# Performance work log

Measured on AMD Instinct MI355X. Metric: run time of the kernel, lower is better.

Reference implementation:

```python
import jax, jax.numpy as jnp
import numpy as np

MAX_ITER = 10
TAU = 1.0


def setup_inputs() -> dict:
    key = jax.random.key(0)
    k1, k2, k3 = jax.random.split(key, 3)
    B, R, C = 64, 1024, 1024
    s = jax.random.normal(k1, (B, R, C), dtype=jnp.float32)
    # nrows <= ncols per batch => no transposed_batch branch in the original
    nrows = jax.random.randint(k2, (B,), 128, 512).astype(jnp.int32)
    ncols = jax.random.randint(k3, (B,), 512, C + 1).astype(jnp.int32)
    return {"s": s, "nrows": nrows, "ncols": ncols}


def _masked_lse(x, mask, axis):
    """logsumexp over `axis` restricted to mask==True; finite-safe everywhere.
    Equivalent to torch.logsumexp after writing -inf into masked-out entries,
    but keeps all values finite so grads are clean."""
    neg = jnp.asarray(-1e30, x.dtype)
    m = jax.lax.stop_gradient(jnp.max(jnp.where(mask, x, neg), axis=axis, keepdims=True))
    e = jnp.where(mask, jnp.exp(jnp.where(mask, x, m) - m), jnp.zeros((), x.dtype))
    sum_e = jnp.sum(e, axis=axis, keepdims=True)
    any_m = jnp.any(mask, axis=axis, keepdims=True)
    return m + jnp.log(jnp.where(any_m, sum_e, jnp.ones((), x.dtype)))


def _sinkhorn(s, nrows, ncols):
    B, R, C = s.shape
    row_mask = (jnp.arange(R)[None, :] < nrows[:, None])[:, :, None]  # [B,R,1]
    col_mask = (jnp.arange(C)[None, :] < ncols[:, None])[:, None, :]  # [B,1,C]
    valid = row_mask & col_mask                                        # [B,R,C]
    log_s = s / TAU
    # Alternating row/col normalization in log space. In the original, entries
    # outside [nrows,ncols] are set to -inf and ignored by logsumexp; here we
    # keep them finite and mask inside the logsumexp, which is the same math
    # on the valid region, and we zero the invalid region at the end (exp(-inf)=0).
    for i in range(MAX_ITER):
        if i % 2 == 0:  # row normalization
            lse = _masked_lse(log_s, valid, axis=2)          # [B,R,1]
            log_s = log_s - jnp.where(row_mask, lse, 0.0)
        else:           # col normalization
            lse = _masked_lse(log_s, valid, axis=1)          # [B,1,C]
            log_s = log_s - jnp.where(col_mask, lse, 0.0)
    return jnp.where(valid, jnp.exp(log_s), jnp.zeros((), s.dtype))


def reference(s, nrows, ncols):
    return _sinkhorn(s, nrows, ncols)
```

## Files before the change

### kernel.cpp

```cpp
#include <hip/hip_runtime.h>
#include <hip/hip_fp16.h>


#define B_DIM 64

__device__ __forceinline__ float fast_rcp(float x) {
#if __has_builtin(__builtin_amdgcn_rcpf)
    return __builtin_amdgcn_rcpf(x);
#else
    return 1.0f / x;
#endif
}

__device__ __forceinline__ float wave_sum(float x) {
    #pragma unroll
    for (int off = 1; off < 64; off <<= 1) x += __shfl_xor(x, off);
    return x;
}


__device__ __forceinline__ void phase2_col(
    const __half* __restrict__ E, const float* a_lds, int b, int r0, int nr,
    int nc, int t, float* __restrict__ cs_cur)
{
    if (r0 >= nr) return;
    const int c0 = t << 1;
    if (c0 >= nc) return;
    const int rend = min(r0 + 64, nr);
    const __half* __restrict__ Eb = E + ((size_t)b << 19) + c0;

    float sA0 = 0.f, sA1 = 0.f, sB0 = 0.f, sB1 = 0.f;
    int r = r0;
    for (; r + 4 <= rend; r += 4) {
        const float2 f0 = __half22float2(*reinterpret_cast<const __half2*>(Eb + ((size_t)(r + 0) << 10)));
        const float2 f1 = __half22float2(*reinterpret_cast<const __half2*>(Eb + ((size_t)(r + 1) << 10)));
        const float2 f2 = __half22float2(*reinterpret_cast<const __half2*>(Eb + ((size_t)(r + 2) << 10)));
        const float2 f3 = __half22float2(*reinterpret_cast<const __half2*>(Eb + ((size_t)(r + 3) << 10)));
        const float a0 = a_lds[r + 0 - r0], a1 = a_lds[r + 1 - r0];
        const float a2 = a_lds[r + 2 - r0], a3 = a_lds[r + 3 - r0];
        sA0 = fmaf(f0.x, a0, sA0); sA1 = fmaf(f0.y, a0, sA1);
        sB0 = fmaf(f1.x, a1, sB0); sB1 = fmaf(f1.y, a1, sB1);
        sA0 = fmaf(f2.x, a2, sA0); sA1 = fmaf(f2.y, a2, sA1);
        sB0 = fmaf(f3.x, a3, sB0); sB1 = fmaf(f3.y, a3, sB1);
    }
    for (; r < rend; ++r) {
        const float2 f = __half22float2(*reinterpret_cast<const __half2*>(Eb + ((size_t)r << 10)));
        const float av = a_lds[r - r0];
        sA0 = fmaf(f.x, av, sA0); sA1 = fmaf(f.y, av, sA1);
    }
    atomicAdd(cs_cur + (b << 10) + c0, sA0 + sB0);
    if (c0 + 1 < nc)
        atomicAdd(cs_cur + (b << 10) + c0 + 1, sA1 + sB1);
}

__global__ __launch_bounds__(512) void pair_first(
    const float* __restrict__ s, const int* __restrict__ nrows,
    const int* __restrict__ ncols, __half* __restrict__ E,
    float* __restrict__ a, float* __restrict__ cs_cur,
    float* __restrict__ cs_next)
{
    const int b = blockIdx.y;
    const int rc = blockIdx.x;
    const int t = threadIdx.x;
    if (t < 128) cs_next[(b << 10) + (rc << 7) + t] = 0.f;

    const int nr = nrows[b];
    const int nc = ncols[b];
    const int r0 = rc << 6;
    __shared__ float a_lds[64];

    const int wave = t >> 6;
    const int lane = t & 63;
    const int cbase = lane << 4;
    const int nv = min(max(nc - cbase, 0), 16);

    if (r0 < nr) {
        #pragma unroll 1
        for (int k = 0; k < 8; ++k) {
            const int r = r0 + (wave << 3) + k;
            float s0 = 0.f, s1 = 0.f;
            if (r < nr) {
                const float* __restrict__ srow =
                    s + ((size_t)b << 20) + ((size_t)r << 10) + cbase;
                __half* __restrict__ erow =
                    E + ((size_t)b << 19) + ((size_t)r << 10) + cbase;
                float e[16];
                #pragma unroll
                for (int q = 0; q < 4; ++q) {
                    const float4 x = *reinterpret_cast<const float4*>(srow + (q << 2));
                    e[4 * q + 0] = __expf(x.x); e[4 * q + 1] = __expf(x.y);
                    e[4 * q + 2] = __expf(x.z); e[4 * q + 3] = __expf(x.w);
                }
                __half2 h[8];
                #pragma unroll
                for (int q = 0; q < 8; ++q)
                    h[q] = __floats2half2_rn(e[2 * q], e[2 * q + 1]);
                *reinterpret_cast<float4*>(erow)     = *reinterpret_cast<float4*>(&h[0]);
                *reinterpret_cast<float4*>(erow + 8) = *reinterpret_cast<float4*>(&h[4]);
                #pragma unroll
                for (int j = 0; j < 16; j += 2) {
                    s0 += (j < nv) ? e[j] : 0.f;
                    s1 += (j + 1 < nv) ? e[j + 1] : 0.f;
                }
            }
            const float sum = wave_sum(s0 + s1);
            if (lane == 0) a_lds[(wave << 3) + k] = (r < nr) ? 1.0f / sum : 0.f;
        }
    } else if (t < 64) {
        a_lds[t] = 0.f;
    }
    __syncthreads();
    if (t < 64) a[(b << 9) + r0 + t] = a_lds[t];

    phase2_col(E, a_lds, b, r0, nr, nc, t, cs_cur);
}

__global__ __launch_bounds__(512) void pair_mid(
    const __half* __restrict__ E, const int* __restrict__ nrows,
    const int* __restrict__ ncols, const float* __restrict__ cs_prev,
    float* __restrict__ a, float* __restrict__ cs_cur,
    float* __restrict__ cs_next)
{
    const int b = blockIdx.y;
    const int rc = blockIdx.x;
    const int t = threadIdx.x;
    if (t < 128) cs_next[(b << 10) + (rc << 7) + t] = 0.f;

    const int nr = nrows[b];
    const int nc = ncols[b];
    const int r0 = rc << 6;
    __shared__ float a_lds[64];

    const int wave = t >> 6;
    const int lane = t & 63;
    const int cbase = lane << 4;

    if (r0 < nr) {
        float w[16];
        const float* __restrict__ csp = cs_prev + (b << 10) + cbase;
        #pragma unroll
        for (int q = 0; q < 4; ++q) {
            const float4 c4 = *reinterpret_cast<const float4*>(csp + (q << 2));
            w[4 * q + 0] = (cbase + 4 * q + 0 < nc) ? fast_rcp(c4.x) : 0.f;
            w[4 * q + 1] = (cbase + 4 * q + 1 < nc) ? fast_rcp(c4.y) : 0.f;
            w[4 * q + 2] = (cbase + 4 * q + 2 < nc) ? fast_rcp(c4.z) : 0.f;
            w[4 * q + 3] = (cbase + 4 * q + 3 < nc) ? fast_rcp(c4.w) : 0.f;
        }
        #pragma unroll 1
        for (int k = 0; k < 8; ++k) {
            const int r = r0 + (wave << 3) + k;
            float s0 = 0.f, s1 = 0.f;
            if (r < nr) {
                const __half* __restrict__ erow =
                    E + ((size_t)b << 19) + ((size_t)r << 10) + cbase;
                float4 p0 = *reinterpret_cast<const float4*>(erow);
                float4 p1 = *reinterpret_cast<const float4*>(erow + 8);
                const __half2* h0 = reinterpret_cast<const __half2*>(&p0);
                const __half2* h1 = reinterpret_cast<const __half2*>(&p1);
                #pragma unroll
                for (int q = 0; q < 4; ++q) {
                    const float2 f = __half22float2(h0[q]);
                    s0 = fmaf(f.x, w[2 * q], s0);
                    s1 = fmaf(f.y, w[2 * q + 1], s1);
                }
                #pragma unroll
                for (int q = 0; q < 4; ++q) {
                    const float2 f = __half22float2(h1[q]);
                    s0 = fmaf(f.x, w[8 + 2 * q], s0);
                    s1 = fmaf(f.y, w[8 + 2 * q + 1], s1);
                }
            }
            const float sum = wave_sum(s0 + s1);
            if (lane == 0) a_lds[(wave << 3) + k] = (r < nr) ? 1.0f / sum : 0.f;
        }
    } else if (t < 64) {
        a_lds[t] = 0.f;
    }
    __syncthreads();
    if (t < 64) a[(b << 9) + r0 + t] = a_lds[t];

    phase2_col(E, a_lds, b, r0, nr, nc, t, cs_cur);
}

__global__ __launch_bounds__(256) void out_step_f(
    const __half* __restrict__ E, const int* __restrict__ nrows,
    const int* __restrict__ ncols, const float* __restrict__ a,
    const float* __restrict__ cs, float* __restrict__ out)
{
    const int g = (blockIdx.x << 8) + threadIdx.x;
    const int b = g >> 18;
    const int rem = g & 262143;
    const int r = rem >> 8;
    const int c0 = (rem & 255) << 2;
    const int nr = nrows[b];
    const int nc = ncols[b];
    float4 o = make_float4(0.f, 0.f, 0.f, 0.f);
    if (r < nr && c0 < nc) {
        const float ar = a[(b << 9) + r];
        float2 pk = *reinterpret_cast<const float2*>(
            E + ((size_t)b << 19) + ((size_t)r << 10) + c0);
        const float2 f01 = __half22float2(reinterpret_cast<const __half2*>(&pk)[0]);
        const float2 f23 = __half22float2(reinterpret_cast<const __half2*>(&pk)[1]);
        const float4 c4 = *reinterpret_cast<const float4*>(cs + (b << 10) + c0);
        o.x = f01.x * ar * fast_rcp(c4.x);
        o.y = (c0 + 1 < nc) ? f01.y * ar * fast_rcp(c4.y) : 0.f;
        o.z = (c0 + 2 < nc) ? f23.x * ar * fast_rcp(c4.z) : 0.f;
        o.w = (c0 + 3 < nc) ? f23.y * ar * fast_rcp(c4.w) : 0.f;
    }
    reinterpret_cast<float4*>(out)[g] = o;
}


__global__ __launch_bounds__(256) void row_step_lg(
    const float* __restrict__ s, const int* __restrict__ nrows,
    const int* __restrict__ ncols, const float* __restrict__ vlog,
    const int use_v, float* __restrict__ u)
{
    const int b = blockIdx.y, r = blockIdx.x;
    const int nr = nrows[b];
    if (r >= nr) return;
    const int nc = ncols[b];
    const int t = threadIdx.x, c0 = t << 2;
    float sum = 0.f;
    if (c0 < nc) {
        const float4 x = reinterpret_cast<const float4*>(
            s + ((size_t)b << 20) + ((size_t)r << 10))[t];
        float4 vv = make_float4(0.f, 0.f, 0.f, 0.f);
        if (use_v) vv = reinterpret_cast<const float4*>(vlog + ((size_t)b << 10))[t];
        sum  = (c0 + 0 < nc) ? __expf(x.x - vv.x) : 0.f;
        sum += (c0 + 1 < nc) ? __expf(x.y - vv.y) : 0.f;
        sum += (c0 + 2 < nc) ? __expf(x.z - vv.z) : 0.f;
        sum += (c0 + 3 < nc) ? __expf(x.w - vv.w) : 0.f;
    }
    #pragma unroll
    for (int off = 1; off < 64; off <<= 1) sum += __shfl_xor(sum, off);
    __shared__ float ss[4];
    if ((t & 63) == 0) ss[t >> 6] = sum;
    __syncthreads();
    if (t == 0) u[((size_t)b << 9) + r] = __logf(ss[0] + ss[1] + ss[2] + ss[3]);
}

__global__ __launch_bounds__(256) void col_step_lg(
    const float* __restrict__ s, const int* __restrict__ nrows,
    const int* __restrict__ ncols, const float* __restrict__ u,
    float* __restrict__ partial)
{
    const int b = blockIdx.z, rc = blockIdx.y;
    const int nr = nrows[b];
    const int r0 = rc << 6;
    if (r0 >= nr) return;
    const int nc = ncols[b];
    const int c = (blockIdx.x << 8) + threadIdx.x;
    float sum = 0.f;
    if (c < nc) {
        const int rend = min(r0 + 64, nr);
        const float* __restrict__ sb = s + ((size_t)b << 20) + c;
        const float* __restrict__ ub = u + ((size_t)b << 9);
        float s0 = 0.f, s1 = 0.f, s2 = 0.f, s3 = 0.f;
        int r = r0;
        for (; r + 4 <= rend; r += 4) {
            s0 += __expf(sb[(size_t)(r + 0) << 10] - ub[r + 0]);
            s1 += __expf(sb[(size_t)(r + 1) << 10] - ub[r + 1]);
            s2 += __expf(sb[(size_t)(r + 2) << 10] - ub[r + 2]);
            s3 += __expf(sb[(size_t)(r + 3) << 10] - ub[r + 3]);
        }
        for (; r < rend; ++r) s0 += __expf(sb[(size_t)r << 10] - ub[r]);
        sum = (s0 + s1) + (s2 + s3);
    }
    partial[(((size_t)b << 3) + rc) << 10 | c] = sum;
}

__global__ __launch_bounds__(256) void col_fin_lg(
    const int* __restrict__ nrows, const float* __restrict__ partial,
    float* __restrict__ vlog)
{
    const int idx = (blockIdx.x << 8) + threadIdx.x;
    const int b = idx >> 10;
    const int nch = (nrows[b] + 63) >> 6;
    const float* __restrict__ p = partial + ((size_t)(b << 3) << 10) + (idx & 1023);
    float sum = 0.f;
    for (int k = 0; k < nch; ++k) sum += p[(size_t)k << 10];
    vlog[idx] = (sum > 0.f) ? __logf(sum) : 0.f;
}

__global__ __launch_bounds__(256) void out_step_lg(
    const float* __restrict__ s, const int* __restrict__ nrows,
    const int* __restrict__ ncols, const float* __restrict__ u,
    const float* __restrict__ vlog, float* __restrict__ out)
{
    const size_t total4 = (size_t)B_DIM * 1024 * 1024 / 4;
    float4* out4 = reinterpret_cast<float4*>(out);
    const float4* s4 = reinterpret_cast<const float4*>(s);
    for (size_t i = (size_t)blockIdx.x * blockDim.x + threadIdx.x; i < total4;
         i += (size_t)gridDim.x * blockDim.x) {
        const int b = (int)(i >> 18);
        const int rem = (int)(i & 262143);
        const int r = rem >> 8;
        const int c0 = (rem & 255) << 2;
        const int nr = nrows[b], nc = ncols[b];
        float4 o;
        if (r >= nr || c0 >= nc) {
            o = make_float4(0.f, 0.f, 0.f, 0.f);
        } else {
            float4 x = s4[i];
            const float ur = u[((size_t)b << 9) + r];
            const float* vb = vlog + ((size_t)b << 10);
            o.x = (c0 + 0 < nc) ? __expf(x.x - ur - vb[c0 + 0]) : 0.f;
            o.y = (c0 + 1 < nc) ? __expf(x.y - ur - vb[c0 + 1]) : 0.f;
            o.z = (c0 + 2 < nc) ? __expf(x.z - ur - vb[c0 + 2]) : 0.f;
            o.w = (c0 + 3 < nc) ? __expf(x.w - ur - vb[c0 + 3]) : 0.f;
        }
        out4[i] = o;
    }
}


extern "C" void kernel_launch(void* const* d_in, const int* in_sizes, int n_in,
                              void* d_out, int out_size, void* d_ws, size_t ws_size,
                              hipStream_t stream) {
    const float* s = (const float*)d_in[0];
    const int* nrows = (const int*)d_in[1];
    const int* ncols = (const int*)d_in[2];
    float* out = (float*)d_out;

    const size_t E_BYTES = (size_t)B_DIM * 512 * 1024 * 2;
    const size_t CS_ELEMS = (size_t)B_DIM * 1024;
    const size_t NEED = E_BYTES + (size_t)B_DIM * 512 * 4 + 3 * CS_ELEMS * 4;

    if (ws_size >= NEED) {
        __half* E = (__half*)d_ws;
        float* a = (float*)((char*)d_ws + E_BYTES);
        float* cs0 = a + B_DIM * 512;
        float* cs1 = cs0 + CS_ELEMS;
        float* cs2 = cs1 + CS_ELEMS;

        hipMemsetAsync(cs0, 0, CS_ELEMS * sizeof(float), stream);

        const dim3 grid(8, B_DIM);
        pair_first<<<grid, 512, 0, stream>>>(s, nrows, ncols, E, a, cs0, cs1);
        pair_mid<<<grid, 512, 0, stream>>>(E, nrows, ncols, cs0, a, cs1, cs2);
        pair_mid<<<grid, 512, 0, stream>>>(E, nrows, ncols, cs1, a, cs2, cs0);
        pair_mid<<<grid, 512, 0, stream>>>(E, nrows, ncols, cs2, a, cs0, cs1);
        pair_mid<<<grid, 512, 0, stream>>>(E, nrows, ncols, cs0, a, cs1, cs2);
        out_step_f<<<65536, 256, 0, stream>>>(E, nrows, ncols, a, cs1, out);
    } else {
        float* u = (float*)d_ws;
        float* vlog = u + (size_t)B_DIM * 512;
        float* partial = vlog + (size_t)B_DIM * 1024;
        const dim3 rowGrid(512, B_DIM);
        const dim3 colGrid(4, 8, B_DIM);
        for (int it = 0; it < 5; ++it) {
            row_step_lg<<<rowGrid, 256, 0, stream>>>(s, nrows, ncols, vlog, it, u);
            col_step_lg<<<colGrid, 256, 0, stream>>>(s, nrows, ncols, u, partial);
            col_fin_lg<<<256, 256, 0, stream>>>(nrows, partial, vlog);
        }
        out_step_lg<<<4096, 256, 0, stream>>>(s, nrows, ncols, u, vlog, out);
    }
}
```

Baseline: 190.6 us.

## Halve row chunk per block and vectorize column reduction with LDS pre-sum

Each block now covers 32 rows instead of 64, which doubles the grid. Blocks with no valid rows exit early. The column-sum phase now has 128 threads, each loading 8 fp16 values in one 16-byte load across 8 rows. The four row-subgroups are summed in LDS, and the result goes to global with atomics that skip zeros. The aim is better occupancy and wider memory loads than the old per-thread 4-byte strided column reads, in exchange for more LDS, an extra barrier, and twice as many atomic flushes per row processed.

```diff
diff --git a/kernel.cpp b/kernel.cpp
--- a/kernel.cpp
+++ b/kernel.cpp
@@ -3,6 +3,8 @@
 
 
 #define B_DIM 64
+#define RCH 32
+#define NCH 16
 
 __device__ __forceinline__ float fast_rcp(float x) {
 #if __has_builtin(__builtin_amdgcn_rcpf)
@@ -18,39 +20,44 @@
     return x;
 }
 
-
 __device__ __forceinline__ void phase2_col(
-    const __half* __restrict__ E, const float* a_lds, int b, int r0, int nr,
-    int nc, int t, float* __restrict__ cs_cur)
-{
-    if (r0 >= nr) return;
-    const int c0 = t << 1;
-    if (c0 >= nc) return;
-    const int rend = min(r0 + 64, nr);
-    const __half* __restrict__ Eb = E + ((size_t)b << 19) + c0;
-
-    float sA0 = 0.f, sA1 = 0.f, sB0 = 0.f, sB1 = 0.f;
-    int r = r0;
-    for (; r + 4 <= rend; r += 4) {
-        const float2 f0 = __half22float2(*reinterpret_cast<const __half2*>(Eb + ((size_t)(r + 0) << 10)));
-        const float2 f1 = __half22float2(*reinterpret_cast<const __half2*>(Eb + ((size_t)(r + 1) << 10)));
-        const float2 f2 = __half22float2(*reinterpret_cast<const __half2*>(Eb + ((size_t)(r + 2) << 10)));
-        const float2 f3 = __half22float2(*reinterpret_cast<const __half2*>(Eb + ((size_t)(r + 3) << 10)));
-        const float a0 = a_lds[r + 0 - r0], a1 = a_lds[r + 1 - r0];
-        const float a2 = a_lds[r + 2 - r0], a3 = a_lds[r + 3 - r0];
-        sA0 = fmaf(f0.x, a0, sA0); sA1 = fmaf(f0.y, a0, sA1);
-        sB0 = fmaf(f1.x, a1, sB0); sB1 = fmaf(f1.y, a1, sB1);
-        sA0 = fmaf(f2.x, a2, sA0); sA1 = fmaf(f2.y, a2, sA1);
-        sB0 = fmaf(f3.x, a3, sB0); sB1 = fmaf(f3.y, a3, sB1);
-    }
-    for (; r < rend; ++r) {
-        const float2 f = __half22float2(*reinterpret_cast<const __half2*>(Eb + ((size_t)r << 10)));
-        const float av = a_lds[r - r0];
-        sA0 = fmaf(f.x, av, sA0); sA1 = fmaf(f.y, av, sA1);
-    }
-    atomicAdd(cs_cur + (b << 10) + c0, sA0 + sB0);
-    if (c0 + 1 < nc)
-        atomicAdd(cs_cur + (b << 10) + c0 + 1, sA1 + sB1);
+    const __half* __restrict__ E, const float* __restrict__ a_lds,
+    float* __restrict__ cls,
+    int b, int r0, int nr, int nc, int t, float* __restrict__ cs_cur)
+{
+    const int c0 = (t & 127) << 3;
+    const int rsub = t >> 7;
+    float acc0 = 0.f, acc1 = 0.f, acc2 = 0.f, acc3 = 0.f;
+    float acc4 = 0.f, acc5 = 0.f, acc6 = 0.f, acc7 = 0.f;
+    if (c0 < nc) {
+        const int rs = r0 + (rsub << 3);
+        const __half* __restrict__ Eb = E + ((size_t)b << 19) + c0;
+        #pragma unroll
+        for (int k = 0; k < 8; ++k) {
+            const int r = rs + k;
+            const float4 p = *reinterpret_cast<const float4*>(Eb + ((size_t)r << 10));
+            const __half2* h = reinterpret_cast<const __half2*>(&p);
+            const float av = a_lds[r - r0];
+            const float2 f0 = __half22float2(h[0]);
+            const float2 f1 = __half22float2(h[1]);
+            const float2 f2 = __half22float2(h[2]);
+            const float2 f3 = __half22float2(h[3]);
+            acc0 = fmaf(f0.x, av, acc0); acc1 = fmaf(f0.y, av, acc1);
+            acc2 = fmaf(f1.x, av, acc2); acc3 = fmaf(f1.y, av, acc3);
+            acc4 = fmaf(f2.x, av, acc4); acc5 = fmaf(f2.y, av, acc5);
+            acc6 = fmaf(f3.x, av, acc6); acc7 = fmaf(f3.y, av, acc7);
+        }
+    }
+    float* dst = cls + (rsub << 10) + c0;
+    *reinterpret_cast<float4*>(dst)     = make_float4(acc0, acc1, acc2, acc3);
+    *reinterpret_cast<float4*>(dst + 4) = make_float4(acc4, acc5, acc6, acc7);
+    __syncthreads();
+    #pragma unroll
+    for (int k = 0; k < 2; ++k) {
+        const int c = t + (k << 9);
+        const float v = cls[c] + cls[1024 + c] + cls[2048 + c] + cls[3072 + c];
+        if (v != 0.f) atomicAdd(cs_cur + (b << 10) + c, v);
+    }
 }
 
 __global__ __launch_bounds__(512) void pair_first(
@@ -62,57 +69,56 @@
     const int b = blockIdx.y;
     const int rc = blockIdx.x;
     const int t = threadIdx.x;
-    if (t < 128) cs_next[(b << 10) + (rc << 7) + t] = 0.f;
-
-    const int nr = nrows[b];
-    const int nc = ncols[b];
-    const int r0 = rc << 6;
-    __shared__ float a_lds[64];
+    if (t < 64) cs_next[(b << 10) + (rc << 6) + t] = 0.f;
+
+    const int nr = nrows[b];
+    const int r0 = rc << 5;
+    if (r0 >= nr) return;
+    const int nc = ncols[b];
+
+    __shared__ float a_lds[RCH];
+    __shared__ float cls[4 * 1024];
 
     const int wave = t >> 6;
     const int lane = t & 63;
     const int cbase = lane << 4;
-    const int nv = min(max(nc - cbase, 0), 16);
-
-    if (r0 < nr) {
-        #pragma unroll 1
-        for (int k = 0; k < 8; ++k) {
-            const int r = r0 + (wave << 3) + k;
-            float s0 = 0.f, s1 = 0.f;
-            if (r < nr) {
-                const float* __restrict__ srow =
-                    s + ((size_t)b << 20) + ((size_t)r << 10) + cbase;
-                __half* __restrict__ erow =
-                    E + ((size_t)b << 19) + ((size_t)r << 10) + cbase;
-                float e[16];
-                #pragma unroll
-                for (int q = 0; q < 4; ++q) {
-                    const float4 x = *reinterpret_cast<const float4*>(srow + (q << 2));
-                    e[4 * q + 0] = __expf(x.x); e[4 * q + 1] = __expf(x.y);
-                    e[4 * q + 2] = __expf(x.z); e[4 * q + 3] = __expf(x.w);
-                }
-                __half2 h[8];
-                #pragma unroll
-                for (int q = 0; q < 8; ++q)
-                    h[q] = __floats2half2_rn(e[2 * q], e[2 * q + 1]);
-                *reinterpret_cast<float4*>(erow)     = *reinterpret_cast<float4*>(&h[0]);
-                *reinterpret_cast<float4*>(erow + 8) = *reinterpret_cast<float4*>(&h[4]);
-                #pragma unroll
-                for (int j = 0; j < 16; j += 2) {
-                    s0 += (j < nv) ? e[j] : 0.f;
-                    s1 += (j + 1 < nv) ? e[j + 1] : 0.f;
-                }
+    const bool cOK = cbase < nc;
+
+    #pragma unroll 1
+    for (int k = 0; k < 4; ++k) {
+        const int r = r0 + (wave << 2) + k;
+        float sum = 0.f;
+        if (r < nr && cOK) {
+            const float* __restrict__ srow =
+                s + ((size_t)b << 20) + ((size_t)r << 10) + cbase;
+            __half* __restrict__ erow =
+                E + ((size_t)b << 19) + ((size_t)r << 10) + cbase;
+            float e[16];
+            #pragma unroll
+            for (int q = 0; q < 4; ++q) {
+                const float4 x = *reinterpret_cast<const float4*>(srow + (q << 2));
+                e[4 * q + 0] = __expf(x.x); e[4 * q + 1] = __expf(x.y);
+                e[4 * q + 2] = __expf(x.z); e[4 * q + 3] = __expf(x.w);
             }
-            const float sum = wave_sum(s0 + s1);
-            if (lane == 0) a_lds[(wave << 3) + k] = (r < nr) ? 1.0f / sum : 0.f;
-        }
-    } else if (t < 64) {
-        a_lds[t] = 0.f;
+            #pragma unroll
+            for (int j = 0; j < 16; ++j)
+                if (cbase + j >= nc) e[j] = 0.f;
+            __half2 h[8];
+            #pragma unroll
+            for (int q = 0; q < 8; ++q)
+                h[q] = __floats2half2_rn(e[2 * q], e[2 * q + 1]);
+            *reinterpret_cast<float4*>(erow)     = *reinterpret_cast<const float4*>(&h[0]);
+            *reinterpret_cast<float4*>(erow + 8) = *reinterpret_cast<const float4*>(&h[4]);
+            #pragma unroll
+            for (int j = 0; j < 16; ++j) sum += e[j];
+        }
+        sum = wave_sum(sum);
+        if (lane == 0) a_lds[(wave << 2) + k] = (r < nr) ? 1.0f / sum : 0.f;
     }
     __syncthreads();
-    if (t < 64) a[(b << 9) + r0 + t] = a_lds[t];
-
-    phase2_col(E, a_lds, b, r0, nr, nc, t, cs_cur);
+    if (t < RCH) a[(b << 9) + r0 + t] = a_lds[t];
+
+    phase2_col(E, a_lds, cls, b, r0, nr, nc, t, cs_cur);
 }
 
 __global__ __launch_bounds__(512) void pair_mid(
@@ -124,19 +130,23 @@
     const int b = blockIdx.y;
     const int rc = blockIdx.x;
     const int t = threadIdx.x;
-    if (t < 128) cs_next[(b << 10) + (rc << 7) + t] = 0.f;
-
-    const int nr = nrows[b];
-    const int nc = ncols[b];
-    const int r0 = rc << 6;
-    __shared__ float a_lds[64];
+    if (t < 64) cs_next[(b << 10) + (rc << 6) + t] = 0.f;
+
+    const int nr = nrows[b];
+    const int r0 = rc << 5;
+    if (r0 >= nr) return;
+    const int nc = ncols[b];
+
+    __shared__ float a_lds[RCH];
+    __shared__ float cls[4 * 1024];
 
     const int wave = t >> 6;
     const int lane = t & 63;
     const int cbase = lane << 4;
-
-    if (r0 < nr) {
-        float w[16];
+    const bool cOK = cbase < nc;
+
+    float w[16];
+    if (cOK) {
         const float* __restrict__ csp = cs_prev + (b << 10) + cbase;
         #pragma unroll
         for (int q = 0; q < 4; ++q) {
@@ -146,40 +156,39 @@
             w[4 * q + 2] = (cbase + 4 * q + 2 < nc) ? fast_rcp(c4.z) : 0.f;
             w[4 * q + 3] = (cbase + 4 * q + 3 < nc) ? fast_rcp(c4.w) : 0.f;
         }
-        #pragma unroll 1
-        for (int k = 0; k < 8; ++k) {
-            const int r = r0 + (wave << 3) + k;
-            float s0 = 0.f, s1 = 0.f;
-            if (r < nr) {
-                const __half* __restrict__ erow =
-                    E + ((size_t)b << 19) + ((size_t)r << 10) + cbase;
-                float4 p0 = *reinterpret_cast<const float4*>(erow);
-                float4 p1 = *reinterpret_cast<const float4*>(erow + 8);
-                const __half2* h0 = reinterpret_cast<const __half2*>(&p0);
-                const __half2* h1 = reinterpret_cast<const __half2*>(&p1);
-                #pragma unroll
-                for (int q = 0; q < 4; ++q) {
-                    const float2 f = __half22float2(h0[q]);
-                    s0 = fmaf(f.x, w[2 * q], s0);
-                    s1 = fmaf(f.y, w[2 * q + 1], s1);
-                }
-                #pragma unroll
-                for (int q = 0; q < 4; ++q) {
-                    const float2 f = __half22float2(h1[q]);
-                    s0 = fmaf(f.x, w[8 + 2 * q], s0);
-                    s1 = fmaf(f.y, w[8 + 2 * q + 1], s1);
-                }
+    }
+
+    #pragma unroll 1
+    for (int k = 0; k < 4; ++k) {
+        const int r = r0 + (wave << 2) + k;
+        float s0 = 0.f, s1 = 0.f;
+        if (r < nr && cOK) {
+            const __half* __restrict__ erow =
+                E + ((size_t)b << 19) + ((size_t)r << 10) + cbase;
+            float4 p0 = *reinterpret_cast<const float4*>(erow);
+            float4 p1 = *reinterpret_cast<const float4*>(erow + 8);
+            const __half2* h0 = reinterpret_cast<const __half2*>(&p0);
+            const __half2* h1 = reinterpret_cast<const __half2*>(&p1);
+            #pragma unroll
+            for (int q = 0; q < 4; ++q) {
+                const float2 f = __half22float2(h0[q]);
+                s0 = fmaf(f.x, w[2 * q], s0);
+                s1 = fmaf(f.y, w[2 * q + 1], s1);
             }
-            const float sum = wave_sum(s0 + s1);
-            if (lane == 0) a_lds[(wave << 3) + k] = (r < nr) ? 1.0f / sum : 0.f;
-        }
-    } else if (t < 64) {
-        a_lds[t] = 0.f;
+            #pragma unroll
+            for (int q = 0; q < 4; ++q) {
+                const float2 f = __half22float2(h1[q]);
+                s0 = fmaf(f.x, w[8 + 2 * q], s0);
+                s1 = fmaf(f.y, w[8 + 2 * q + 1], s1);
+            }
+        }
+        const float sum = wave_sum(s0 + s1);
+        if (lane == 0) a_lds[(wave << 2) + k] = (r < nr) ? 1.0f / sum : 0.f;
     }
     __syncthreads();
-    if (t < 64) a[(b << 9) + r0 + t] = a_lds[t];
-
-    phase2_col(E, a_lds, b, r0, nr, nc, t, cs_cur);
+    if (t < RCH) a[(b << 9) + r0 + t] = a_lds[t];
+
+    phase2_col(E, a_lds, cls, b, r0, nr, nc, t, cs_cur);
 }
 
 __global__ __launch_bounds__(256) void out_step_f(
@@ -336,7 +345,7 @@
 
         hipMemsetAsync(cs0, 0, CS_ELEMS * sizeof(float), stream);
 
-        const dim3 grid(8, B_DIM);
+        const dim3 grid(NCH, B_DIM);
         pair_first<<<grid, 512, 0, stream>>>(s, nrows, ncols, E, a, cs0, cs1);
         pair_mid<<<grid, 512, 0, stream>>>(E, nrows, ncols, cs0, a, cs1, cs2);
         pair_mid<<<grid, 512, 0, stream>>>(E, nrows, ncols, cs1, a, cs2, cs0);
```

Result: faster. 161.4 us (-15.3%).
